# Performance work log

Measured on AMD Instinct MI355X. Metric: run time of the kernel, lower is better.

The kernel has to match this reference:

```python
import jax, jax.numpy as jnp
import numpy as np
from math import sqrt

DIM = 2048
N_HEADS = 2
HEAD_DIM = DIM // N_HEADS  # 1024 == RoPE dims (dim // 2)
ROPE_DIMS = DIM // 2
ROPE_BASE = 10000.0


def apply_rope(x, dims=ROPE_DIMS, base=ROPE_BASE, offset=0):
    # x: [B, H, L, Dh]; non-traditional (split-half) RoPE over sequence axis
    L = x.shape[-2]
    pos = jnp.arange(offset, offset + L, dtype=x.dtype)[:, None]          # [L,1]
    inv = jnp.exp(jnp.arange(0, dims, 2, dtype=x.dtype) * (-np.log(base) / dims))  # [dims//2]
    theta = pos * inv                                                      # [L, dims//2]
    cos, sin = jnp.cos(theta), jnp.sin(theta)
    h = dims // 2
    x1, x2 = x[..., :h], x[..., h:dims]
    rx1 = x1 * cos - x2 * sin
    rx2 = x1 * sin + x2 * cos
    if dims < x.shape[-1]:
        return jnp.concatenate([rx1, rx2, x[..., dims:]], axis=-1)
    return jnp.concatenate([rx1, rx2], axis=-1)


def setup_inputs() -> dict:
    key = jax.random.key(0)
    ks = jax.random.split(key, 6)
    B, L = 4, 2048
    x = jax.random.normal(ks[0], (B, L, DIM), dtype=jnp.float32)
    # causal additive mask
    causal = jnp.tril(jnp.ones((L, L), dtype=bool))
    mask = jnp.where(causal, 0.0, -1e9).astype(jnp.float32)
    s1 = 1.0 / sqrt(DIM)
    Wqkv_w = jax.random.normal(ks[1], (3 * DIM, DIM), dtype=jnp.float32) * s1
    Wqkv_b = jnp.zeros((3 * DIM,), dtype=jnp.float32)
    out_w = jax.random.normal(ks[2], (DIM, DIM), dtype=jnp.float32) * s1
    out_b = jnp.zeros((DIM,), dtype=jnp.float32)
    return {"x": x, "mask": mask, "Wqkv_w": Wqkv_w, "Wqkv_b": Wqkv_b,
            "out_w": out_w, "out_b": out_b}


def reference(x, mask, Wqkv_w, Wqkv_b, out_w, out_b):
    B, L, D = x.shape
    H, Dh = N_HEADS, HEAD_DIM
    qkv = x @ Wqkv_w.T + Wqkv_b                       # [B, L, 3D]
    q, k, v = jnp.split(qkv, 3, axis=-1)
    # b l (h d) -> b h l d
    split = lambda t: t.reshape(B, L, H, Dh).transpose(0, 2, 1, 3)
    q, k, v = split(q), split(k), split(v)
    q = apply_rope(q)
    k = apply_rope(k)
    scale = sqrt(1.0 / Dh)
    scores = jnp.einsum('bhld,bhkd->bhlk', q * scale, k)  # [B,H,L,L]
    scores = scores + mask                                 # additive causal mask
    probs = jax.nn.softmax(scores, axis=-1)
    vh = jnp.einsum('bhlk,bhkd->bhld', probs, v)
    vh = vh.transpose(0, 2, 1, 3).reshape(B, L, D)         # b h l d -> b l (h d)
    out = vh @ out_w.T + out_b
    return (out, k, v)
```

## Files before the change

kernel.cpp:

```cpp
#include <hip/hip_runtime.h>
#include <hip/hip_bf16.h>
#include <math.h>

typedef unsigned short u16;
typedef __attribute__((ext_vector_type(8))) __bf16 bf16x8;
typedef __attribute__((ext_vector_type(4))) float f32x4;

__device__ __forceinline__ u16 f2b(float f) {
  unsigned u = __builtin_bit_cast(unsigned, f);
  u += 0x7fffu + ((u >> 16) & 1u);
  return (u16)(u >> 16);
}
__device__ __forceinline__ float b2f(u16 h) {
  unsigned u = ((unsigned)h) << 16;
  return __builtin_bit_cast(float, u);
}

__device__ __forceinline__ void gld_lds16(const u16* g, u16* l) {
  __builtin_amdgcn_global_load_lds(
      (const __attribute__((address_space(1))) unsigned int*)g,
      (__attribute__((address_space(3))) unsigned int*)l, 16, 0, 0);
}

#define MFMA16(a, b, c) \
  c = __builtin_amdgcn_mfma_f32_16x16x32_bf16(a, b, c, 0, 0, 0)

template <class FC>
__device__ __forceinline__ void gemm128_body(const u16* A, int lda,
                                             const u16* B, int ldb, FC fc,
                                             int m0, int n0, int K) {
  __shared__ __align__(16) u16 As[128 * 64];
  __shared__ __align__(16) u16 Bs[128 * 64];
  const int tid = threadIdx.x;
  const int wave = tid >> 6;
  const int lane = tid & 63;
  const int srow = lane >> 3;
  const int scol = ((lane & 7) ^ srow) * 8;
  const int wm = (wave & 1) * 64;
  const int wn = (wave >> 1) * 64;
  const int fm = lane & 15;
  const int fs = fm & 7;

  const u16* Abase = A + (size_t)m0 * lda;
  const u16* Bbase = B + (size_t)n0 * ldb;
  const size_t aLane = (size_t)(wave * 8 + srow) * lda + scol;
  const size_t bLane = (size_t)(wave * 8 + srow) * ldb + scol;

  f32x4 acc[4][4];
#pragma unroll
  for (int i = 0; i < 4; ++i)
#pragma unroll
    for (int j = 0; j < 4; ++j) acc[i][j] = (f32x4){0.f, 0.f, 0.f, 0.f};

  for (int k0 = 0; k0 < K; k0 += 64) {
#pragma unroll
    for (int c = 0; c < 4; ++c) {
      gld_lds16(Abase + (aLane + (size_t)(c * 32) * lda + k0),
                &As[(c * 4 + wave) * 512]);
      gld_lds16(Bbase + (bLane + (size_t)(c * 32) * ldb + k0),
                &Bs[(c * 4 + wave) * 512]);
    }
    __syncthreads();
#pragma unroll
    for (int kk = 0; kk < 2; ++kk) {
      const int cb = kk * 4 + (lane >> 4);
      const int p8 = (cb ^ fs) * 8;
      bf16x8 af[4], bfr[4];
#pragma unroll
      for (int i = 0; i < 4; ++i)
        af[i] = *(const bf16x8*)&As[(wm + i * 16 + fm) * 64 + p8];
#pragma unroll
      for (int j = 0; j < 4; ++j)
        bfr[j] = *(const bf16x8*)&Bs[(wn + j * 16 + fm) * 64 + p8];
#pragma unroll
      for (int i = 0; i < 4; ++i)
#pragma unroll
        for (int j = 0; j < 4; ++j) MFMA16(af[i], bfr[j], acc[i][j]);
    }
    __syncthreads();
  }
  const int er = lane >> 4;
#pragma unroll
  for (int i = 0; i < 4; ++i)
#pragma unroll
    for (int j = 0; j < 4; ++j)
#pragma unroll
      for (int r = 0; r < 4; ++r) {
        int m = m0 + wm + i * 16 + er * 4 + r;
        int n = n0 + wn + j * 16 + fm;
        fc(m, n, acc[i][j][r]);
      }
}

template <class FC>
__device__ __forceinline__ void gemm256_body(const u16* A, int lda,
                                             const u16* B, int ldb, FC fc,
                                             int m0, int n0, int K) {
  __shared__ __align__(16) u16 As[2][16384];
  __shared__ __align__(16) u16 Bs[2][16384];
  const int tid = threadIdx.x;
  const int wave = tid >> 6;
  const int lane = tid & 63;
  const int wr = wave >> 2;
  const int wc = wave & 3;
  const int fm = lane & 15;
  const int cb4 = lane >> 4;
  const int fs = fm & 7;
  const int srow = lane >> 3;
  const int scol = ((lane & 7) ^ srow) * 8;

  const u16* Ab = A + (size_t)(m0 + srow) * lda + scol;
  const u16* Bb = B + (size_t)(n0 + srow) * ldb + scol;

  const int paRow = (wr * 128 + fm) * 64;
  const int pbRow = (wc * 64 + fm) * 64;
  const int q0 = (cb4 ^ fs) * 8;
  const int q1 = q0 ^ 32;

  f32x4 acc[8][4];
#pragma unroll
  for (int m = 0; m < 8; ++m)
#pragma unroll
    for (int n = 0; n < 4; ++n) acc[m][n] = (f32x4){0.f, 0.f, 0.f, 0.f};

  auto stA2 = [&](int bi, int kg) {
#pragma unroll
    for (int h = 0; h < 2; ++h) {
      const u16* g = Ab + (size_t)(h * 128 + wave * 8) * lda + kg;
      gld_lds16(g, &As[bi][h * 8192 + wave * 512]);
      gld_lds16(g + (size_t)64 * lda, &As[bi][h * 8192 + (wave + 8) * 512]);
    }
  };
  auto stB2 = [&](int bi, int kg) {
#pragma unroll
    for (int h = 0; h < 2; ++h) {
      const u16* g = Bb + (size_t)(h * 128 + wave * 8) * ldb + kg;
      gld_lds16(g, &Bs[bi][h * 8192 + wave * 512]);
      gld_lds16(g + (size_t)64 * ldb, &Bs[bi][h * 8192 + (wave + 8) * 512]);
    }
  };

  const int nkt = K >> 6;

  stB2(0, 0);
  stA2(0, 0);
  stB2(1, 64);
  stA2(1, 64);
  asm volatile("s_waitcnt vmcnt(8)" ::: "memory");
  __builtin_amdgcn_s_barrier();
  bf16x8 af[8], bv[4][2];
#pragma unroll
  for (int m = 0; m < 8; ++m)
    af[m] = *(const bf16x8*)&As[0][paRow + m * 1024 + q0];
#pragma unroll
  for (int n = 0; n < 4; ++n) {
    bv[n][0] = *(const bf16x8*)&Bs[0][pbRow + n * 1024 + q0];
    bv[n][1] = *(const bf16x8*)&Bs[0][pbRow + n * 1024 + q1];
  }
  asm volatile("s_waitcnt lgkmcnt(0)" ::: "memory");
  __builtin_amdgcn_s_barrier();

  int buf = 0;
  for (int T = 0; T < nkt; ++T, buf ^= 1) {
    const int kc = T * 64;
    const bool sA1 = (T + 1) < nkt;
    const bool sN2 = (T + 2) < nkt;
    if (sN2) stB2(buf, kc + 128);
    __builtin_amdgcn_sched_barrier(0);
    __builtin_amdgcn_s_setprio(1);
#pragma unroll
    for (int m = 0; m < 8; ++m) {
      MFMA16(af[m], bv[0][0], acc[m][0]);
      MFMA16(af[m], bv[1][0], acc[m][1]);
      MFMA16(af[m], bv[2][0], acc[m][2]);
      MFMA16(af[m], bv[3][0], acc[m][3]);
      af[m] = *(const bf16x8*)&As[buf][paRow + m * 1024 + q1];
      __builtin_amdgcn_sched_group_barrier(0x008, 4, 0);
      __builtin_amdgcn_sched_group_barrier(0x100, 1, 0);
    }
    __builtin_amdgcn_s_setprio(0);
    asm volatile("s_waitcnt lgkmcnt(0)" ::: "memory");
    __builtin_amdgcn_s_barrier();
    if (sN2) stA2(buf, kc + 128);
    __builtin_amdgcn_sched_barrier(0);
    if (sN2) {
      asm volatile("s_waitcnt vmcnt(8)" ::: "memory");
    } else if (sA1) {
      asm volatile("s_waitcnt vmcnt(0)" ::: "memory");
    }
    __builtin_amdgcn_s_barrier();
    __builtin_amdgcn_s_setprio(1);
    if (sA1) {
#pragma unroll
      for (int m = 0; m < 4; ++m) {
        MFMA16(af[m], bv[0][1], acc[m][0]);
        MFMA16(af[m], bv[1][1], acc[m][1]);
        MFMA16(af[m], bv[2][1], acc[m][2]);
        MFMA16(af[m], bv[3][1], acc[m][3]);
        af[m] = *(const bf16x8*)&As[buf ^ 1][paRow + m * 1024 + q0];
        bv[m][0] = *(const bf16x8*)&Bs[buf ^ 1][pbRow + m * 1024 + q0];
        __builtin_amdgcn_sched_group_barrier(0x008, 4, 0);
        __builtin_amdgcn_sched_group_barrier(0x100, 2, 0);
      }
#pragma unroll
      for (int m = 4; m < 8; ++m) {
        MFMA16(af[m], bv[0][1], acc[m][0]);
        MFMA16(af[m], bv[1][1], acc[m][1]);
        MFMA16(af[m], bv[2][1], acc[m][2]);
        MFMA16(af[m], bv[3][1], acc[m][3]);
        af[m] = *(const bf16x8*)&As[buf ^ 1][paRow + m * 1024 + q0];
        __builtin_amdgcn_sched_group_barrier(0x008, 4, 0);
        __builtin_amdgcn_sched_group_barrier(0x100, 1, 0);
      }
#pragma unroll
      for (int n = 0; n < 4; ++n)
        bv[n][1] = *(const bf16x8*)&Bs[buf ^ 1][pbRow + n * 1024 + q1];
    } else {
#pragma unroll
      for (int m = 0; m < 8; ++m) {
        MFMA16(af[m], bv[0][1], acc[m][0]);
        MFMA16(af[m], bv[1][1], acc[m][1]);
        MFMA16(af[m], bv[2][1], acc[m][2]);
        MFMA16(af[m], bv[3][1], acc[m][3]);
      }
    }
    __builtin_amdgcn_s_setprio(0);
    asm volatile("s_waitcnt lgkmcnt(0)" ::: "memory");
    __builtin_amdgcn_s_barrier();
  }

  const int er = lane >> 4;
#pragma unroll
  for (int m = 0; m < 8; ++m)
#pragma unroll
    for (int n = 0; n < 4; ++n)
#pragma unroll
      for (int r = 0; r < 4; ++r)
        fc(m0 + wr * 128 + m * 16 + er * 4 + r, n0 + wc * 64 + n * 16 + fm,
           acc[m][n][r]);
}

struct EQKV {
  u16* qb;
  u16* kb;
  float* vout;
  const float* bias;
  __device__ __forceinline__ void operator()(int m, int n, float v) const {
    v += bias[n];
    int b = m >> 11, l = m & 2047;
    int part = n >> 11, nn = n & 2047, h = nn >> 10, d = nn & 1023;
    size_t idx = ((size_t)((b << 1) + h) * 2048 + l) * 1024 + d;
    if (part == 0)
      qb[idx] = f2b(v);
    else if (part == 1)
      kb[idx] = f2b(v);
    else
      vout[idx] = v;
  }
};
struct EScoreB {
  u16* S;
  __device__ __forceinline__ void operator()(int m, int n, float v) const {
    S[((size_t)m << 11) + n] = f2b(v * 0.03125f + (n > m ? -1.0e9f : 0.0f));
  }
};
struct EBf16 {
  u16* o;
  int ld;
  __device__ __forceinline__ void operator()(int m, int n, float v) const {
    o[(size_t)m * ld + n] = f2b(v);
  }
};
struct EOut {
  float* o;
  const float* bias;
  __device__ __forceinline__ void operator()(int m, int n, float v) const {
    o[((size_t)m << 11) + n] = v + bias[n];
  }
};

__device__ __forceinline__ u16* spz(u16* sp0, u16* sp1, int z) {
  return (z < 4) ? sp0 + (size_t)z * 4194304 : sp1 + (size_t)(z - 4) * 4194304;
}

__global__ void __launch_bounds__(256) k_cast3(const float* x, const float* w1,
                                               const float* w2, u16* xb,
                                               u16* w1b, u16* w2b) {
  long i = (long)(blockIdx.x * 256 + threadIdx.x) * 4;
  const float* src;
  u16* dst;
  long off;
  if (i < 16777216L) {
    src = x; dst = xb; off = i;
  } else if (i < 16777216L + 12582912L) {
    src = w1; dst = w1b; off = i - 16777216L;
  } else {
    src = w2; dst = w2b; off = i - 16777216L - 12582912L;
  }
  float4 f = *(const float4*)(src + off);
  ushort4 o;
  o.x = f2b(f.x);
  o.y = f2b(f.y);
  o.z = f2b(f.z);
  o.w = f2b(f.w);
  *(ushort4*)(dst + off) = o;
}

__global__ void __launch_bounds__(512, 2) k_qkv(const u16* xb, const u16* wb,
                                                const float* bias, u16* qb,
                                                u16* kb, float* vout) {
  gemm256_body(xb, 2048, wb, 2048, EQKV{qb, kb, vout, bias}, blockIdx.y * 256,
               blockIdx.x * 256, 2048);
}

__global__ void __launch_bounds__(256) k_rope(u16* qb, u16* kb, float* kout) {
  int l = blockIdx.x;
  int t = threadIdx.x;
  float lf = (float)l;
  const float c0 = (float)(-9.210340371976184 / 1024.0);
  float sa, ca, sb, cb;
  {
    float inva = __expf((float)(4 * t) * c0);
    __sincosf(lf * inva, &sa, &ca);
    float invb = __expf((float)(4 * t + 2) * c0);
    __sincosf(lf * invb, &sb, &cb);
  }
  const int d = 2 * t;
#pragma unroll
  for (int bh = 0; bh < 8; ++bh) {
    size_t base = ((size_t)bh * 2048 + l) * 1024;
    ushort2 x1 = *(const ushort2*)&qb[base + d];
    ushort2 x2 = *(const ushort2*)&qb[base + 512 + d];
    float a1 = b2f(x1.x), a2 = b2f(x2.x);
    float b1 = b2f(x1.y), b2 = b2f(x2.y);
    ushort2 q1 = {f2b(a1 * ca - a2 * sa), f2b(b1 * cb - b2 * sb)};
    ushort2 q2 = {f2b(a1 * sa + a2 * ca), f2b(b1 * sb + b2 * cb)};
    *(ushort2*)&qb[base + d] = q1;
    *(ushort2*)&qb[base + 512 + d] = q2;
    ushort2 y1 = *(const ushort2*)&kb[base + d];
    ushort2 y2 = *(const ushort2*)&kb[base + 512 + d];
    float k1a = b2f(y1.x), k2a = b2f(y2.x);
    float k1b = b2f(y1.y), k2b = b2f(y2.y);
    float r1a = k1a * ca - k2a * sa, r2a = k1a * sa + k2a * ca;
    float r1b = k1b * cb - k2b * sb, r2b = k1b * sb + k2b * cb;
    ushort2 ka = {f2b(r1a), f2b(r1b)};
    ushort2 kc = {f2b(r2a), f2b(r2b)};
    *(ushort2*)&kb[base + d] = ka;
    *(ushort2*)&kb[base + 512 + d] = kc;
    *(float2*)&kout[base + d] = make_float2(r1a, r1b);
    *(float2*)&kout[base + 512 + d] = make_float2(r2a, r2b);
  }
}

__global__ void __launch_bounds__(256) k_transpose_v(const float* v, u16* vt) {
  __shared__ u16 tile[64][65];
  int bh = blockIdx.z;
  int d0 = blockIdx.x * 64, l0 = blockIdx.y * 64;
  const float* vb = v + (size_t)bh * 2048 * 1024;
  u16* vtb = vt + (size_t)bh * 1024 * 2048;
  int t = threadIdx.x;
  int c = t & 63, r4 = t >> 6;
#pragma unroll
  for (int r = 0; r < 16; ++r) {
    int row = r * 4 + r4;
    tile[row][c] = f2b(vb[(size_t)(l0 + row) * 1024 + d0 + c]);
  }
  __syncthreads();
#pragma unroll
  for (int r = 0; r < 16; ++r) {
    int drow = r * 4 + r4;
    vtb[(size_t)(d0 + drow) * 2048 + l0 + c] = tile[c][drow];
  }
}

__global__ void __launch_bounds__(256) k_score(const u16* qb, const u16* kb,
                                               u16* sp0, u16* sp1) {
  int m0 = blockIdx.y * 128, n0 = blockIdx.x * 128;
  if (n0 > m0) return;
  int z = blockIdx.z;
  const u16* q = qb + (size_t)z * 2048 * 1024;
  const u16* k = kb + (size_t)z * 2048 * 1024;
  gemm128_body(q, 1024, k, 1024, EScoreB{spz(sp0, sp1, z)}, m0, n0, 1024);
}

__global__ void __launch_bounds__(256) k_softmax(u16* sp0, u16* sp1) {
  int l = blockIdx.x, z = blockIdx.y;
  u16* row = spz(sp0, sp1, z) + ((size_t)l << 11);
  int t = threadIdx.x;
  int jend = ((l >> 8) + 1) << 8;
  __shared__ float red[4];
  float vals[8];
  float mx = -1e30f;
#pragma unroll
  for (int i = 0; i < 8; ++i) {
    int j = i * 256 + t;
    float v = (j <= l) ? b2f(row[j]) : -1e30f;
    vals[i] = v;
    mx = fmaxf(mx, v);
  }
#pragma unroll
  for (int off = 32; off; off >>= 1) mx = fmaxf(mx, __shfl_down(mx, off));
  if ((t & 63) == 0) red[t >> 6] = mx;
  __syncthreads();
  mx = fmaxf(fmaxf(red[0], red[1]), fmaxf(red[2], red[3]));
  __syncthreads();
  float sum = 0.f;
#pragma unroll
  for (int i = 0; i < 8; ++i) {
    int j = i * 256 + t;
    float e = (j <= l) ? __expf(vals[i] - mx) : 0.f;
    vals[i] = e;
    sum += e;
  }
#pragma unroll
  for (int off = 32; off; off >>= 1) sum += __shfl_down(sum, off);
  if ((t & 63) == 0) red[t >> 6] = sum;
  __syncthreads();
  sum = red[0] + red[1] + red[2] + red[3];
  float is = 1.0f / sum;
#pragma unroll
  for (int i = 0; i < 8; ++i) {
    int j = i * 256 + t;
    if (j < jend) row[j] = f2b(vals[i] * is);
  }
}

__global__ void __launch_bounds__(256) k_pv(u16* sp0, u16* sp1, const u16* vt,
                                            u16* vh) {
  int z = blockIdx.z;
  int b = z >> 1, h = z & 1;
  int m0 = blockIdx.y * 128, n0 = blockIdx.x * 128;
  const u16* Pz = spz(sp0, sp1, z);
  const u16* vtb = vt + (size_t)z * 1024 * 2048;
  u16* outb = vh + (size_t)b * 2048 * 2048 + (size_t)h * 1024;
  int Keff = m0 + 128;
  gemm128_body(Pz, 2048, vtb, 2048, EBf16{outb, 2048}, m0, n0, Keff);
}

__global__ void __launch_bounds__(512, 2) k_out(const u16* vh, const u16* w2,
                                                const float* bias, float* out) {
  gemm256_body(vh, 2048, w2, 2048, EOut{out, bias}, blockIdx.y * 256,
               blockIdx.x * 256, 2048);
}

extern "C" void kernel_launch(void* const* d_in, const int* in_sizes, int n_in,
                              void* d_out, int out_size, void* d_ws,
                              size_t ws_size, hipStream_t stream) {
  const float* x = (const float*)d_in[0];
  const float* w1 = (const float*)d_in[2];
  const float* b1 = (const float*)d_in[3];
  const float* w2 = (const float*)d_in[4];
  const float* b2 = (const float*)d_in[5];
  float* out = (float*)d_out;
  float* kout = out + (size_t)16777216;
  float* vout = kout + (size_t)16777216;

  char* ws = (char*)d_ws;
  u16* xb = (u16*)ws;
  ws += (size_t)33554432;
  u16* w1b = (u16*)ws;
  ws += (size_t)25165824;
  u16* w2b = (u16*)ws;
  ws += (size_t)8388608;
  u16* qb = (u16*)ws;
  ws += (size_t)33554432;
  u16* kb = (u16*)ws;
  ws += (size_t)33554432;
  u16* vtb = (u16*)ws;
  ws += (size_t)33554432;
  u16* sp1 = (u16*)ws;
  u16* sp0 = xb;
  u16* vh = qb;

  k_cast3<<<32768, 256, 0, stream>>>(x, w1, w2, xb, w1b, w2b);
  k_qkv<<<dim3(24, 32), 512, 0, stream>>>(xb, w1b, b1, qb, kb, vout);
  k_rope<<<2048, 256, 0, stream>>>(qb, kb, kout);
  k_transpose_v<<<dim3(16, 32, 8), 256, 0, stream>>>(vout, vtb);
  k_score<<<dim3(16, 16, 8), 256, 0, stream>>>(qb, kb, sp0, sp1);
  k_softmax<<<dim3(2048, 8), 256, 0, stream>>>(sp0, sp1);
  k_pv<<<dim3(8, 16, 8), 256, 0, stream>>>(sp0, sp1, vtb, vh);
  k_out<<<dim3(8, 32), 512, 0, stream>>>(vh, w2b, b2, out);
}
```

Before: 782.9 us.

## Restructure GEMM main loop into four quadrant phases with interleaved half-tile prefetch

Rewrites the 256x256 bf16 GEMM main loop so each K-tile is processed in four quadrant phases, with A/B fragments read from LDS just in time. Global-to-LDS loads are split into half-tiles and issued between the phases, replacing the earlier scheme that kept whole-tile fragments in registers across iterations. The aim is lower register pressure and finer-grained overlap of loads with MFMA work, at the cost of more barriers per iteration and less explicit MFMA/LDS interleaving.

```diff
diff --git a/kernel.cpp b/kernel.cpp
--- a/kernel.cpp
+++ b/kernel.cpp
@@ -123,109 +123,125 @@
 #pragma unroll
     for (int n = 0; n < 4; ++n) acc[m][n] = (f32x4){0.f, 0.f, 0.f, 0.f};
 
-  auto stA2 = [&](int bi, int kg) {
-#pragma unroll
-    for (int h = 0; h < 2; ++h) {
-      const u16* g = Ab + (size_t)(h * 128 + wave * 8) * lda + kg;
-      gld_lds16(g, &As[bi][h * 8192 + wave * 512]);
-      gld_lds16(g + (size_t)64 * lda, &As[bi][h * 8192 + (wave + 8) * 512]);
-    }
+  auto stA = [&](int bi, int h, int kg) {
+    const u16* g = Ab + (size_t)(h * 128 + wave * 8) * lda + kg;
+    gld_lds16(g, &As[bi][h * 8192 + wave * 512]);
+    gld_lds16(g + (size_t)64 * lda, &As[bi][h * 8192 + (wave + 8) * 512]);
   };
-  auto stB2 = [&](int bi, int kg) {
-#pragma unroll
-    for (int h = 0; h < 2; ++h) {
-      const u16* g = Bb + (size_t)(h * 128 + wave * 8) * ldb + kg;
-      gld_lds16(g, &Bs[bi][h * 8192 + wave * 512]);
-      gld_lds16(g + (size_t)64 * ldb, &Bs[bi][h * 8192 + (wave + 8) * 512]);
-    }
+  auto stB = [&](int bi, int h, int kg) {
+    const u16* g = Bb + (size_t)(h * 128 + wave * 8) * ldb + kg;
+    gld_lds16(g, &Bs[bi][h * 8192 + wave * 512]);
+    gld_lds16(g + (size_t)64 * ldb, &Bs[bi][h * 8192 + (wave + 8) * 512]);
   };
 
   const int nkt = K >> 6;
 
-  stB2(0, 0);
-  stA2(0, 0);
-  stB2(1, 64);
-  stA2(1, 64);
-  asm volatile("s_waitcnt vmcnt(8)" ::: "memory");
-  __builtin_amdgcn_s_barrier();
-  bf16x8 af[8], bv[4][2];
-#pragma unroll
-  for (int m = 0; m < 8; ++m)
-    af[m] = *(const bf16x8*)&As[0][paRow + m * 1024 + q0];
-#pragma unroll
-  for (int n = 0; n < 4; ++n) {
-    bv[n][0] = *(const bf16x8*)&Bs[0][pbRow + n * 1024 + q0];
-    bv[n][1] = *(const bf16x8*)&Bs[0][pbRow + n * 1024 + q1];
-  }
-  asm volatile("s_waitcnt lgkmcnt(0)" ::: "memory");
+  stB(0, 0, 0);
+  stA(0, 0, 0);
+  stA(0, 1, 0);
+  stB(0, 1, 0);
+  stB(1, 0, 64);
+  stA(1, 0, 64);
+  asm volatile("s_waitcnt vmcnt(4)" ::: "memory");
   __builtin_amdgcn_s_barrier();
 
   int buf = 0;
   for (int T = 0; T < nkt; ++T, buf ^= 1) {
     const int kc = T * 64;
-    const bool sA1 = (T + 1) < nkt;
-    const bool sN2 = (T + 2) < nkt;
-    if (sN2) stB2(buf, kc + 128);
+    const bool sT1 = (T + 1) < nkt;
+    const bool sT2 = (T + 2) < nkt;
+    bf16x8 a0[4], a1[4], b0[4], b1[4];
+#pragma unroll
+    for (int m = 0; m < 4; ++m) {
+      a0[m] = *(const bf16x8*)&As[buf][paRow + m * 1024 + q0];
+      a1[m] = *(const bf16x8*)&As[buf][paRow + m * 1024 + q1];
+    }
+#pragma unroll
+    for (int n = 0; n < 2; ++n) {
+      b0[n] = *(const bf16x8*)&Bs[buf][pbRow + n * 1024 + q0];
+      b1[n] = *(const bf16x8*)&Bs[buf][pbRow + n * 1024 + q1];
+    }
+    if (sT1) stA(buf ^ 1, 1, kc + 64);
+    asm volatile("s_waitcnt lgkmcnt(8)" ::: "memory");
+    __builtin_amdgcn_s_barrier();
+    asm volatile("s_waitcnt lgkmcnt(0)" ::: "memory");
     __builtin_amdgcn_sched_barrier(0);
     __builtin_amdgcn_s_setprio(1);
 #pragma unroll
-    for (int m = 0; m < 8; ++m) {
-      MFMA16(af[m], bv[0][0], acc[m][0]);
-      MFMA16(af[m], bv[1][0], acc[m][1]);
-      MFMA16(af[m], bv[2][0], acc[m][2]);
-      MFMA16(af[m], bv[3][0], acc[m][3]);
-      af[m] = *(const bf16x8*)&As[buf][paRow + m * 1024 + q1];
-      __builtin_amdgcn_sched_group_barrier(0x008, 4, 0);
-      __builtin_amdgcn_sched_group_barrier(0x100, 1, 0);
+    for (int m = 0; m < 4; ++m) {
+      MFMA16(a0[m], b0[0], acc[m][0]);
+      MFMA16(a0[m], b0[1], acc[m][1]);
+    }
+#pragma unroll
+    for (int m = 0; m < 4; ++m) {
+      MFMA16(a1[m], b1[0], acc[m][0]);
+      MFMA16(a1[m], b1[1], acc[m][1]);
     }
     __builtin_amdgcn_s_setprio(0);
+    __builtin_amdgcn_s_barrier();
+#pragma unroll
+    for (int n = 2; n < 4; ++n) {
+      b0[n] = *(const bf16x8*)&Bs[buf][pbRow + n * 1024 + q0];
+      b1[n] = *(const bf16x8*)&Bs[buf][pbRow + n * 1024 + q1];
+    }
+    if (sT1) stB(buf ^ 1, 1, kc + 64);
+    __builtin_amdgcn_s_barrier();
     asm volatile("s_waitcnt lgkmcnt(0)" ::: "memory");
-    __builtin_amdgcn_s_barrier();
-    if (sN2) stA2(buf, kc + 128);
     __builtin_amdgcn_sched_barrier(0);
-    if (sN2) {
-      asm volatile("s_waitcnt vmcnt(8)" ::: "memory");
-    } else if (sA1) {
+    __builtin_amdgcn_s_setprio(1);
+#pragma unroll
+    for (int m = 0; m < 4; ++m) {
+      MFMA16(a0[m], b0[2], acc[m][2]);
+      MFMA16(a0[m], b0[3], acc[m][3]);
+    }
+#pragma unroll
+    for (int m = 0; m < 4; ++m) {
+      MFMA16(a1[m], b1[2], acc[m][2]);
+      MFMA16(a1[m], b1[3], acc[m][3]);
+    }
+    __builtin_amdgcn_s_setprio(0);
+    __builtin_amdgcn_s_barrier();
+#pragma unroll
+    for (int m = 0; m < 4; ++m) {
+      a0[m] = *(const bf16x8*)&As[buf][paRow + (m + 4) * 1024 + q0];
+      a1[m] = *(const bf16x8*)&As[buf][paRow + (m + 4) * 1024 + q1];
+    }
+    if (sT2) stB(buf, 0, kc + 128);
+    __builtin_amdgcn_s_barrier();
+    asm volatile("s_waitcnt lgkmcnt(0)" ::: "memory");
+    __builtin_amdgcn_sched_barrier(0);
+    __builtin_amdgcn_s_setprio(1);
+#pragma unroll
+    for (int m = 0; m < 4; ++m) {
+      MFMA16(a0[m], b0[0], acc[m + 4][0]);
+      MFMA16(a0[m], b0[1], acc[m + 4][1]);
+    }
+#pragma unroll
+    for (int m = 0; m < 4; ++m) {
+      MFMA16(a1[m], b1[0], acc[m + 4][0]);
+      MFMA16(a1[m], b1[1], acc[m + 4][1]);
+    }
+    __builtin_amdgcn_s_setprio(0);
+    __builtin_amdgcn_s_barrier();
+    if (sT2) stA(buf, 0, kc + 128);
+    __builtin_amdgcn_s_barrier();
+    __builtin_amdgcn_s_setprio(1);
+#pragma unroll
+    for (int m = 0; m < 4; ++m) {
+      MFMA16(a0[m], b0[2], acc[m + 4][2]);
+      MFMA16(a0[m], b0[3], acc[m + 4][3]);
+    }
+#pragma unroll
+    for (int m = 0; m < 4; ++m) {
+      MFMA16(a1[m], b1[2], acc[m + 4][2]);
+      MFMA16(a1[m], b1[3], acc[m + 4][3]);
+    }
+    __builtin_amdgcn_s_setprio(0);
+    if (sT2) {
+      asm volatile("s_waitcnt vmcnt(4)" ::: "memory");
+    } else if (sT1) {
       asm volatile("s_waitcnt vmcnt(0)" ::: "memory");
     }
-    __builtin_amdgcn_s_barrier();
-    __builtin_amdgcn_s_setprio(1);
-    if (sA1) {
-#pragma unroll
-      for (int m = 0; m < 4; ++m) {
-        MFMA16(af[m], bv[0][1], acc[m][0]);
-        MFMA16(af[m], bv[1][1], acc[m][1]);
-        MFMA16(af[m], bv[2][1], acc[m][2]);
-        MFMA16(af[m], bv[3][1], acc[m][3]);
-        af[m] = *(const bf16x8*)&As[buf ^ 1][paRow + m * 1024 + q0];
-        bv[m][0] = *(const bf16x8*)&Bs[buf ^ 1][pbRow + m * 1024 + q0];
-        __builtin_amdgcn_sched_group_barrier(0x008, 4, 0);
-        __builtin_amdgcn_sched_group_barrier(0x100, 2, 0);
-      }
-#pragma unroll
-      for (int m = 4; m < 8; ++m) {
-        MFMA16(af[m], bv[0][1], acc[m][0]);
-        MFMA16(af[m], bv[1][1], acc[m][1]);
-        MFMA16(af[m], bv[2][1], acc[m][2]);
-        MFMA16(af[m], bv[3][1], acc[m][3]);
-        af[m] = *(const bf16x8*)&As[buf ^ 1][paRow + m * 1024 + q0];
-        __builtin_amdgcn_sched_group_barrier(0x008, 4, 0);
-        __builtin_amdgcn_sched_group_barrier(0x100, 1, 0);
-      }
-#pragma unroll
-      for (int n = 0; n < 4; ++n)
-        bv[n][1] = *(const bf16x8*)&Bs[buf ^ 1][pbRow + n * 1024 + q1];
-    } else {
-#pragma unroll
-      for (int m = 0; m < 8; ++m) {
-        MFMA16(af[m], bv[0][1], acc[m][0]);
-        MFMA16(af[m], bv[1][1], acc[m][1]);
-        MFMA16(af[m], bv[2][1], acc[m][2]);
-        MFMA16(af[m], bv[3][1], acc[m][3]);
-      }
-    }
-    __builtin_amdgcn_s_setprio(0);
-    asm volatile("s_waitcnt lgkmcnt(0)" ::: "memory");
     __builtin_amdgcn_s_barrier();
   }
 
```

Result: slower. 809.5 us (+3.4%).
